# Kernel optimization log

Hardware: AMD Instinct MI355X
Metric: run time of the kernel (lower is better)

The kernel has to match this reference:

```python
import jax, jax.numpy as jnp
import numpy as np
from jax.ops import segment_sum, segment_max

N, E, FIN, H, C, L, G, ED = 50000, 400000, 256, 4, 64, 3, 25, 2
D = H * C  # 256 = dim*heads


def setup_inputs() -> dict:
    key = jax.random.key(0)
    k = jax.random.split(key, 16)
    s = 0.05
    f = jnp.float32
    return {
        "x": jax.random.normal(k[0], (N, FIN), f),
        "edge_attr": jax.random.uniform(k[1], (E, ED), dtype=f),
        "edge_index": jax.random.randint(k[2], (2, E), 0, N),
        "batch": jnp.sort(jax.random.randint(k[3], (N,), 0, G)),
        "W_pre": jax.random.normal(k[4], (FIN, D), f) * s,
        "b_pre": jnp.zeros((D,), f),
        "W_src": jax.random.normal(k[5], (L, D, D), f) * s,
        "W_dst": jax.random.normal(k[6], (L, D, D), f) * s,
        "W_edge": jax.random.normal(k[7], (L, ED, D), f) * s,
        "att_src": jax.random.normal(k[8], (L, H, C), f) * s,
        "att_dst": jax.random.normal(k[9], (L, H, C), f) * s,
        "att_edge": jax.random.normal(k[10], (L, H, C), f) * s,
        "bias_conv": jnp.zeros((L, D), f),
        "ln_gamma": jnp.ones((L, D), f),
        "ln_beta": jnp.zeros((L, D), f),
        "prelu_a": jnp.full((L, D), 0.25, f),
        "W_post1": jax.random.normal(k[11], (D * (L + 1), D), f) * s,
        "b_post1": jnp.zeros((D,), f),
        "W_post2": jax.random.normal(k[12], (D, D), f) * s,
        "b_post2": jnp.zeros((D,), f),
        "W_risk": jax.random.normal(k[13], (D, 1), f) * s,
        "b_risk": jnp.zeros((1,), f),
    }


def _segment_mean(v, seg, num):
    tot = segment_sum(v, seg, num_segments=num)
    cnt = segment_sum(jnp.ones((v.shape[0], 1), v.dtype), seg, num_segments=num)
    return tot / jnp.maximum(cnt, 1.0)


def _layer_norm(h, g, b, eps=1e-5):
    mu = jnp.mean(h, -1, keepdims=True)
    var = jnp.var(h, -1, keepdims=True)
    return (h - mu) * jax.lax.rsqrt(var + eps) * g + b


def _gat_forward(x, edge_attr, edge_index, batch, params):
    (W_pre, b_pre, W_src, W_dst, W_edge, att_src, att_dst, att_edge,
     bias_conv, ln_gamma, ln_beta, prelu_a,
     W_post1, b_post1, W_post2, b_post2, W_risk, b_risk) = params
    row, col = edge_index[0], edge_index[1]  # src -> dst
    # preprocess: project raw node features to D = dim*heads
    h = x @ W_pre + b_pre  # [N, D]
    concat = [_segment_mean(h, batch, G)]  # x0_glob
    for l in range(L):  # fixed small layer count
        xs = (h @ W_src[l]).reshape(N, H, C)
        xd = (h @ W_dst[l]).reshape(N, H, C)
        ea = (edge_attr @ W_edge[l]).reshape(E, H, C)
        # edge-wise attention logits [E, H]
        a = ((xs * att_src[l]).sum(-1)[row]
             + (xd * att_dst[l]).sum(-1)[col]
             + (ea * att_edge[l]).sum(-1))
        a = jax.nn.leaky_relu(a, 0.2)
        # segment softmax over destination nodes
        m = segment_max(a, col, num_segments=N)
        w = jnp.exp(a - m[col])
        z = segment_sum(w, col, num_segments=N)
        alpha = w / (z[col] + 1e-16)  # [E, H]
        # weighted message passing: gather src feats, scatter-add to dst
        out = segment_sum(xs[row] * alpha[:, :, None], col, num_segments=N)
        out = out.reshape(N, D) + bias_conv[l]
        # per-graph LayerNorm loop == single row-wise LayerNorm
        out = _layer_norm(out, ln_gamma[l], ln_beta[l])
        # channel-wise PReLU
        out = jnp.where(out > 0, out, prelu_a[l] * out)
        concat.append(_segment_mean(out, batch, G))
        h = out + h  # residual_connection == 'Y'
    xc = jnp.concatenate(concat, axis=1)  # [G, D*(L+1)]
    p = jax.nn.relu(xc @ W_post1 + b_post1)
    p = jax.nn.relu(p @ W_post2 + b_post2)
    return p @ W_risk + b_risk  # [G, 1] risk


def reference(x, edge_attr, edge_index, batch, W_pre, b_pre, W_src, W_dst,
              W_edge, att_src, att_dst, att_edge, bias_conv, ln_gamma,
              ln_beta, prelu_a, W_post1, b_post1, W_post2, b_post2,
              W_risk, b_risk):
    params = (W_pre, b_pre, W_src, W_dst, W_edge, att_src, att_dst, att_edge,
              bias_conv, ln_gamma, ln_beta, prelu_a,
              W_post1, b_post1, W_post2, b_post2, W_risk, b_risk)
    return _gat_forward(x, edge_attr, edge_index, batch, params)
```

## Files before the change

kernel.cpp:

```cpp
#include <hip/hip_runtime.h>
#include <math.h>

#define NN 50000
#define NPAD 50048
#define EE 400000
#define DD 256
#define HH 4
#define CC 64
#define LL 3
#define GG 25

typedef _Float16 half4_t __attribute__((ext_vector_type(4)));
typedef _Float16 half8_t __attribute__((ext_vector_type(8)));
typedef float f32x4_t __attribute__((ext_vector_type(4)));

__global__ __launch_bounds__(256) void gemm_mfma(
    const _Float16* __restrict__ Ahi, const _Float16* __restrict__ Alo,
    const _Float16* __restrict__ Bhi, const _Float16* __restrict__ Blo,
    const float* __restrict__ bias, float* __restrict__ C, int N)
{
  __shared__ _Float16 lds[4][128][32];
  const int t = threadIdx.x;
  const int wave = t >> 6, lane = t & 63;
  const int m0 = blockIdx.x * 128, bn0 = blockIdx.y * 128;
  const int wm = wave >> 1, wn = wave & 1;

  f32x4_t acc[4][4];
#pragma unroll
  for (int i = 0; i < 4; i++)
#pragma unroll
    for (int j = 0; j < 4; j++) acc[i][j] = (f32x4_t){0.f, 0.f, 0.f, 0.f};

  const int l15 = lane & 15, kg = lane >> 4;
  int aoff[4], boff[4];
#pragma unroll
  for (int tr = 0; tr < 4; tr++) {
    int r = wm * 64 + tr * 16 + l15;
    aoff[tr] = r * 64 + ((kg ^ ((r >> 1) & 3)) * 16);
    int n = wn * 64 + tr * 16 + l15;
    boff[tr] = n * 64 + ((kg ^ ((n >> 1) & 3)) * 16);
  }

  const _Float16* gsrc[4];
  gsrc[0] = Ahi + (size_t)m0 * 256;
  gsrc[1] = Alo + (size_t)m0 * 256;
  gsrc[2] = Bhi + (size_t)bn0 * 256;
  gsrc[3] = Blo + (size_t)bn0 * 256;

  const char* lbase = (const char*)&lds[0][0][0];

  for (int k0 = 0; k0 < DD; k0 += 32) {
    __syncthreads();
#pragma unroll
    for (int b = 0; b < 4; b++) {
#pragma unroll
      for (int c = 0; c < 2; c++) {
        int rowbase = (wave << 5) + (c << 4);
        const _Float16* g = gsrc[b] + (size_t)(rowbase + (lane >> 2)) * 256
                            + k0 + (lane & 3) * 8;
        char* l = (char*)lbase + b * 8192 + rowbase * 64;
        __builtin_amdgcn_global_load_lds(
            (const __attribute__((address_space(1))) void*)g,
            (__attribute__((address_space(3))) void*)l, 16, 0, 0);
      }
    }
    __syncthreads();

    half8_t ah[4], al[4], bh[4], bl[4];
#pragma unroll
    for (int i = 0; i < 4; i++) {
      ah[i] = *(const half8_t*)(lbase + 0 * 8192 + aoff[i]);
      al[i] = *(const half8_t*)(lbase + 1 * 8192 + aoff[i]);
      bh[i] = *(const half8_t*)(lbase + 2 * 8192 + boff[i]);
      bl[i] = *(const half8_t*)(lbase + 3 * 8192 + boff[i]);
    }
#pragma unroll
    for (int i = 0; i < 4; i++)
#pragma unroll
      for (int j = 0; j < 4; j++) {
        acc[i][j] = __builtin_amdgcn_mfma_f32_16x16x32_f16(ah[i], bh[j], acc[i][j], 0, 0, 0);
        acc[i][j] = __builtin_amdgcn_mfma_f32_16x16x32_f16(ah[i], bl[j], acc[i][j], 0, 0, 0);
        acc[i][j] = __builtin_amdgcn_mfma_f32_16x16x32_f16(al[i], bh[j], acc[i][j], 0, 0, 0);
      }
  }

#pragma unroll
  for (int i = 0; i < 4; i++) {
    int rb = m0 + wm * 64 + i * 16 + (lane >> 4) * 4;
#pragma unroll
    for (int j = 0; j < 4; j++) {
      int col = bn0 + wn * 64 + j * 16 + l15;
      float bv = bias ? bias[col] : 0.f;
#pragma unroll
      for (int q = 0; q < 4; q++) {
        int r = rb + q;
        if (r < N) C[(size_t)r * DD + col] = acc[i][j][q] + bv;
      }
    }
  }
}

__global__ __launch_bounds__(256) void split_f16(
    const float* __restrict__ src, _Float16* __restrict__ hi,
    _Float16* __restrict__ lo, int N)
{
  int f = blockIdx.x * 256 + threadIdx.x;
  if (f >= N * 64) return;
  int m = f >> 6, q = f & 63;
  float4 v = *(const float4*)(src + (size_t)f * 4);
  int gp = (q >> 1) ^ ((m >> 1) & 3);
  int off = m * 256 + gp * 8 + (q & 1) * 4;
  half4_t h4, l4;
  h4[0] = (_Float16)v.x; l4[0] = (_Float16)(v.x - (float)h4[0]);
  h4[1] = (_Float16)v.y; l4[1] = (_Float16)(v.y - (float)h4[1]);
  h4[2] = (_Float16)v.z; l4[2] = (_Float16)(v.z - (float)h4[2]);
  h4[3] = (_Float16)v.w; l4[3] = (_Float16)(v.w - (float)h4[3]);
  *(half4_t*)(hi + off) = h4;
  *(half4_t*)(lo + off) = l4;
}

__global__ void prep_w(const float* __restrict__ W, _Float16* __restrict__ bhi,
                       _Float16* __restrict__ blo)
{
  int n = blockIdx.x, k = threadIdx.x;
  float v = W[(size_t)k * DD + n];
  _Float16 h = (_Float16)v, l = (_Float16)(v - (float)h);
  int kp = (((k >> 3) ^ ((n >> 1) & 3)) << 3) | (k & 7);
  bhi[(size_t)n * DD + kp] = h;
  blo[(size_t)n * DD + kp] = l;
}

__global__ void prep_att(const float* __restrict__ Ws, const float* __restrict__ Wd,
                         const float* __restrict__ We, const float* __restrict__ as_,
                         const float* __restrict__ ad_, const float* __restrict__ ae_,
                         float* __restrict__ wmat, float* __restrict__ wea)
{
  int l = blockIdx.x;
  int t = threadIdx.x;
  for (int idx = t; idx < DD * 8; idx += 256) {
    int k = idx >> 3, hd = idx & 7;
    const float* W; const float* att; int hh;
    if (hd < 4) { W = Ws; att = as_; hh = hd; }
    else        { W = Wd; att = ad_; hh = hd - 4; }
    const float* wrow = W + (size_t)l * DD * DD + (size_t)k * DD + hh * CC;
    const float* arow = att + l * DD + hh * CC;
    float s = 0.f;
#pragma unroll 4
    for (int c = 0; c < CC; c++) s = fmaf(wrow[c], arow[c], s);
    wmat[(size_t)l * DD * 8 + idx] = s;
  }
  if (t < 8) {
    int d = t >> 2, hh = t & 3;
    const float* wrow = We + (size_t)l * 2 * DD + (size_t)d * DD + hh * CC;
    const float* arow = ae_ + l * DD + hh * CC;
    float s = 0.f;
#pragma unroll 4
    for (int c = 0; c < CC; c++) s = fmaf(wrow[c], arow[c], s);
    wea[l * 8 + d * 4 + hh] = s;
  }
}

__global__ void graph_bounds(const int* __restrict__ batch, int* __restrict__ goff,
                             int N, int G)
{
  int g = threadIdx.x;
  if (g > G) return;
  int lo = 0, hi = N;
  while (lo < hi) { int mid = (lo + hi) >> 1; if (batch[mid] < g) lo = mid + 1; else hi = mid; }
  goff[g] = lo;
}

__global__ void hist_col(const int* __restrict__ ei, int* __restrict__ deg, int E)
{
  int e = blockIdx.x * 256 + threadIdx.x;
  if (e < E) atomicAdd(&deg[ei[E + e]], 1);
}

__global__ void scan1(const int* __restrict__ deg, int* __restrict__ incl,
                      int* __restrict__ bsum, int N)
{
  __shared__ int sm[256];
  int b = blockIdx.x, t = threadIdx.x;
  int i = b * 256 + t;
  int v = (i < N) ? deg[i] : 0;
  sm[t] = v;
  __syncthreads();
  for (int off = 1; off < 256; off <<= 1) {
    int add = (t >= off) ? sm[t - off] : 0;
    __syncthreads();
    sm[t] += add;
    __syncthreads();
  }
  if (i < N) incl[i] = sm[t];
  if (t == 255) bsum[b] = sm[255];
}

__global__ void scan2(int* __restrict__ bsum, int nb)
{
  if (threadIdx.x == 0 && blockIdx.x == 0) {
    int run = 0;
    for (int i = 0; i < nb; i++) { int v = bsum[i]; bsum[i] = run; run += v; }
  }
}

__global__ void scan3(const int* __restrict__ deg, const int* __restrict__ incl,
                      const int* __restrict__ bsum, int* __restrict__ rowptr,
                      int* __restrict__ cur, int N, int E)
{
  int i = blockIdx.x * 256 + threadIdx.x;
  if (i < N) {
    int ex = incl[i] - deg[i] + bsum[blockIdx.x];
    rowptr[i] = ex;
    cur[i] = ex;
  }
  if (i == 0) rowptr[N] = E;
}

__global__ void scatter_edges(const int* __restrict__ ei, const float* __restrict__ eattr,
                              int* __restrict__ cur, int* __restrict__ srow,
                              float2* __restrict__ sea, int E)
{
  int e = blockIdx.x * 256 + threadIdx.x;
  if (e < E) {
    int c = ei[E + e];
    int p = atomicAdd(&cur[c], 1);
    srow[p] = ei[e];
    sea[p] = ((const float2*)eattr)[e];
  }
}

__global__ __launch_bounds__(256) void att_proj(
    const float* __restrict__ h, const float* __restrict__ wmatL,
    float* __restrict__ asrc, float* __restrict__ adst, int N)
{
  __shared__ float Hs[32][260];
  __shared__ float Wm[DD * 8];
  int t = threadIdx.x;
  for (int i = t; i < DD * 8; i += 256) Wm[i] = wmatL[i];
  int n0 = blockIdx.x * 32;
  for (int i = t; i < 32 * 64; i += 256) {
    int n = i >> 6, c4 = i & 63;
    float4 v = {0.f, 0.f, 0.f, 0.f};
    if (n0 + n < N) v = *(const float4*)(h + (size_t)(n0 + n) * DD + c4 * 4);
    Hs[n][c4 * 4 + 0] = v.x; Hs[n][c4 * 4 + 1] = v.y;
    Hs[n][c4 * 4 + 2] = v.z; Hs[n][c4 * 4 + 3] = v.w;
  }
  __syncthreads();
  int n = t >> 3, hd = t & 7;
  float s0 = 0, s1 = 0, s2 = 0, s3 = 0;
  for (int k = 0; k < DD; k += 4) {
    s0 = fmaf(Hs[n][k + 0], Wm[(k + 0) * 8 + hd], s0);
    s1 = fmaf(Hs[n][k + 1], Wm[(k + 1) * 8 + hd], s1);
    s2 = fmaf(Hs[n][k + 2], Wm[(k + 2) * 8 + hd], s2);
    s3 = fmaf(Hs[n][k + 3], Wm[(k + 3) * 8 + hd], s3);
  }
  float s = (s0 + s1) + (s2 + s3);
  int gn = n0 + n;
  if (gn < N) {
    if (hd < 4) asrc[gn * 4 + hd] = s;
    else        adst[gn * 4 + (hd - 4)] = s;
  }
}

__global__ __launch_bounds__(256) void dst_fused(
    const float* __restrict__ xs, const float* __restrict__ asrc,
    const float* __restrict__ adst, const int* __restrict__ rowptr,
    const int* __restrict__ srow, const float2* __restrict__ sea,
    const float* __restrict__ weaL, const float* __restrict__ biasL,
    const float* __restrict__ gL, const float* __restrict__ bL,
    const float* __restrict__ pL, float* __restrict__ h,
    _Float16* __restrict__ hhi, _Float16* __restrict__ hlo, int N)
{
  int wid = blockIdx.x * 4 + (threadIdx.x >> 6);
  int lane = threadIdx.x & 63;
  if (wid >= N) return;
  const int head = lane >> 4;
  const int start = rowptr[wid];
  const int end = rowptr[wid + 1];
  const float ad = adst[wid * 4 + head];
  const float w0 = weaL[head];
  const float w1 = weaL[4 + head];
  float ax = 0.f, ay = 0.f, az = 0.f, aw = 0.f;
  float z = 0.f;
  int p = start;
  for (; p + 2 <= end; p += 2) {
    int r0 = srow[p], r1 = srow[p + 1];
    float2 e0 = sea[p], e1 = sea[p + 1];
    float s0 = asrc[r0 * 4 + head], s1 = asrc[r1 * 4 + head];
    float4 x0 = *(const float4*)(xs + (size_t)r0 * DD + lane * 4);
    float4 x1 = *(const float4*)(xs + (size_t)r1 * DD + lane * 4);
    float a0 = s0 + ad + e0.x * w0 + e0.y * w1;
    a0 = a0 > 0.f ? a0 : 0.2f * a0;
    float wt0 = expf(a0);
    float a1 = s1 + ad + e1.x * w0 + e1.y * w1;
    a1 = a1 > 0.f ? a1 : 0.2f * a1;
    float wt1 = expf(a1);
    z += wt0 + wt1;
    ax = fmaf(wt0, x0.x, ax); ay = fmaf(wt0, x0.y, ay);
    az = fmaf(wt0, x0.z, az); aw = fmaf(wt0, x0.w, aw);
    ax = fmaf(wt1, x1.x, ax); ay = fmaf(wt1, x1.y, ay);
    az = fmaf(wt1, x1.z, az); aw = fmaf(wt1, x1.w, aw);
  }
  if (p < end) {
    int r = srow[p];
    float2 ea = sea[p];
    float a = asrc[r * 4 + head] + ad + ea.x * w0 + ea.y * w1;
    a = a > 0.f ? a : 0.2f * a;
    float wt = expf(a);
    z += wt;
    float4 xv = *(const float4*)(xs + (size_t)r * DD + lane * 4);
    ax = fmaf(wt, xv.x, ax); ay = fmaf(wt, xv.y, ay);
    az = fmaf(wt, xv.z, az); aw = fmaf(wt, xv.w, aw);
  }
  float inv = 1.f / (z + 1e-16f);
  float4 bi = *(const float4*)(biasL + lane * 4);
  float o0 = ax * inv + bi.x;
  float o1 = ay * inv + bi.y;
  float o2 = az * inv + bi.z;
  float o3 = aw * inv + bi.w;
  float s = (o0 + o1) + (o2 + o3);
  float q = (o0 * o0 + o1 * o1) + (o2 * o2 + o3 * o3);
#pragma unroll
  for (int off = 32; off; off >>= 1) {
    s += __shfl_xor(s, off, 64);
    q += __shfl_xor(q, off, 64);
  }
  float mu = s * (1.f / 256.f);
  float var = q * (1.f / 256.f) - mu * mu;
  float rs = rsqrtf(var + 1e-5f);
  float4 gg = *(const float4*)(gL + lane * 4);
  float4 bb = *(const float4*)(bL + lane * 4);
  float4 pp = *(const float4*)(pL + lane * 4);
  o0 = (o0 - mu) * rs * gg.x + bb.x;  o0 = o0 > 0.f ? o0 : pp.x * o0;
  o1 = (o1 - mu) * rs * gg.y + bb.y;  o1 = o1 > 0.f ? o1 : pp.y * o1;
  o2 = (o2 - mu) * rs * gg.z + bb.z;  o2 = o2 > 0.f ? o2 : pp.z * o2;
  o3 = (o3 - mu) * rs * gg.w + bb.w;  o3 = o3 > 0.f ? o3 : pp.w * o3;
  float4 hv = *(const float4*)(h + (size_t)wid * DD + lane * 4);
  float4 ov;
  ov.x = o0 + hv.x; ov.y = o1 + hv.y; ov.z = o2 + hv.z; ov.w = o3 + hv.w;
  *(float4*)(h + (size_t)wid * DD + lane * 4) = ov;
  if (hhi) {
    int gp = (lane >> 1) ^ ((wid >> 1) & 3);
    int off2 = wid * DD + gp * 8 + (lane & 1) * 4;
    half4_t h4, l4;
    h4[0] = (_Float16)ov.x; l4[0] = (_Float16)(ov.x - (float)h4[0]);
    h4[1] = (_Float16)ov.y; l4[1] = (_Float16)(ov.y - (float)h4[1]);
    h4[2] = (_Float16)ov.z; l4[2] = (_Float16)(ov.z - (float)h4[2]);
    h4[3] = (_Float16)ov.w; l4[3] = (_Float16)(ov.w - (float)h4[3]);
    *(half4_t*)(hhi + off2) = h4;
    *(half4_t*)(hlo + off2) = l4;
  }
}

__global__ void mean_accum(const float* __restrict__ x, const int* __restrict__ goff,
                           float* __restrict__ msum)
{
  int g = blockIdx.x, sp = blockIdx.y, t = threadIdx.x;
  int lo = goff[g], hi = goff[g + 1];
  int cnt = hi - lo;
  if (cnt <= 0) return;
  int per = (cnt + gridDim.y - 1) / gridDim.y;
  int st = lo + sp * per;
  int en = min(hi, st + per);
  if (st >= en) return;
  float acc = 0.f;
  for (int n = st; n < en; ++n) acc += x[(size_t)n * DD + t];
  atomicAdd(&msum[g * DD + t], acc);
}

__global__ void mean_fin(const float* __restrict__ msum, const int* __restrict__ goff,
                         float* __restrict__ dst)
{
  int g = blockIdx.x, t = threadIdx.x;
  int cnt = goff[g + 1] - goff[g];
  dst[g * DD + t] = msum[g * DD + t] / fmaxf((float)cnt, 1.f);
}

__global__ __launch_bounds__(256) void head_mlp(
    const float* __restrict__ hmean, const float* __restrict__ W1,
    const float* __restrict__ b1, const float* __restrict__ W2,
    const float* __restrict__ b2, const float* __restrict__ Wr,
    const float* __restrict__ br, float* __restrict__ out)
{
  __shared__ float xc[4 * DD];
  __shared__ float p1[DD];
  __shared__ float red[256];
  int g = blockIdx.x, t = threadIdx.x;
  float m0 = hmean[0 * GG * DD + g * DD + t];
  float m1 = hmean[1 * GG * DD + g * DD + t];
  float m2 = hmean[2 * GG * DD + g * DD + t];
  float m3 = hmean[3 * GG * DD + g * DD + t];
  xc[t] = m0;
  xc[DD + t] = m1 - m0;
  xc[2 * DD + t] = m2 - m1;
  xc[3 * DD + t] = m3 - m2;
  __syncthreads();
  float acc = b1[t];
  for (int k = 0; k < 4 * DD; k++) acc = fmaf(xc[k], W1[(size_t)k * DD + t], acc);
  p1[t] = fmaxf(acc, 0.f);
  __syncthreads();
  float acc2 = b2[t];
  for (int k = 0; k < DD; k++) acc2 = fmaf(p1[k], W2[(size_t)k * DD + t], acc2);
  float v = fmaxf(acc2, 0.f) * Wr[t];
  red[t] = v;
  __syncthreads();
  for (int sdown = 128; sdown; sdown >>= 1) {
    if (t < sdown) red[t] += red[t + sdown];
    __syncthreads();
  }
  if (t == 0) out[g] = red[0] + br[0];
}

extern "C" void kernel_launch(void* const* d_in, const int* in_sizes, int n_in,
                              void* d_out, int out_size, void* d_ws, size_t ws_size,
                              hipStream_t stream)
{
  const float* x        = (const float*)d_in[0];
  const float* eattr    = (const float*)d_in[1];
  const int*   eidx     = (const int*)d_in[2];
  const int*   batch    = (const int*)d_in[3];
  const float* W_pre    = (const float*)d_in[4];
  const float* b_pre    = (const float*)d_in[5];
  const float* W_src    = (const float*)d_in[6];
  const float* W_dst    = (const float*)d_in[7];
  const float* W_edge   = (const float*)d_in[8];
  const float* att_src  = (const float*)d_in[9];
  const float* att_dst  = (const float*)d_in[10];
  const float* att_edge = (const float*)d_in[11];
  const float* bias_conv= (const float*)d_in[12];
  const float* ln_g     = (const float*)d_in[13];
  const float* ln_b     = (const float*)d_in[14];
  const float* prelu    = (const float*)d_in[15];
  const float* W1       = (const float*)d_in[16];
  const float* b1       = (const float*)d_in[17];
  const float* W2       = (const float*)d_in[18];
  const float* b2       = (const float*)d_in[19];
  const float* Wr       = (const float*)d_in[20];
  const float* br       = (const float*)d_in[21];
  float* out = (float*)d_out;

  char* w = (char*)d_ws;
  size_t off = 0;
  auto alloc = [&](size_t bytes) -> char* {
    char* p = w + off;
    off += (bytes + 255) & ~(size_t)255;
    return p;
  };
  float*     h     = (float*)alloc((size_t)NN * DD * 4);
  char*      xsreg = alloc((size_t)NPAD * DD * 4);
  float*     xs    = (float*)xsreg;
  _Float16*  x_hi  = (_Float16*)xsreg;
  _Float16*  x_lo  = (_Float16*)(xsreg + (size_t)NPAD * DD * 2);
  _Float16*  h_hi  = (_Float16*)alloc((size_t)NPAD * DD * 2);
  _Float16*  h_lo  = (_Float16*)alloc((size_t)NPAD * DD * 2);
  _Float16*  bt_hi = (_Float16*)alloc((size_t)4 * DD * DD * 2);
  _Float16*  bt_lo = (_Float16*)alloc((size_t)4 * DD * DD * 2);
  float*  asrc  = (float*)alloc((size_t)NN * HH * 4);
  float*  adst  = (float*)alloc((size_t)NN * HH * 4);
  float*  wmat  = (float*)alloc((size_t)LL * DD * 8 * 4);
  float*  wea   = (float*)alloc((size_t)LL * 8 * 4);
  float*  hmean = (float*)alloc((size_t)(LL + 1) * GG * DD * 4);
  float*  msum  = (float*)alloc((size_t)GG * DD * 4);
  float2* sea   = (float2*)alloc((size_t)EE * 8);
  int*    goff  = (int*)alloc((GG + 1) * 4);
  int*    deg   = (int*)alloc((size_t)NN * 4);
  int*    rowptr= (int*)alloc((size_t)(NN + 1) * 4);
  int*    cur   = (int*)alloc((size_t)NN * 4);
  int*    incl  = (int*)alloc((size_t)NN * 4);
  int*    bsum  = (int*)alloc(256 * 4);
  int*    srow  = (int*)alloc((size_t)EE * 4);
  if (off > ws_size) return;

  prep_att<<<dim3(LL), dim3(256), 0, stream>>>(W_src, W_dst, W_edge, att_src,
                                               att_dst, att_edge, wmat, wea);
  prep_w<<<dim3(DD), dim3(DD), 0, stream>>>(W_pre, bt_hi, bt_lo);
  for (int l = 0; l < LL; l++)
    prep_w<<<dim3(DD), dim3(DD), 0, stream>>>(W_src + (size_t)l * DD * DD,
                                              bt_hi + (size_t)(l + 1) * DD * DD,
                                              bt_lo + (size_t)(l + 1) * DD * DD);
  graph_bounds<<<dim3(1), dim3(32), 0, stream>>>(batch, goff, NN, GG);
  hipMemsetAsync(deg, 0, (size_t)NN * 4, stream);
  hist_col<<<dim3((EE + 255) / 256), dim3(256), 0, stream>>>(eidx, deg, EE);
  int nb = (NN + 255) / 256;
  scan1<<<dim3(nb), dim3(256), 0, stream>>>(deg, incl, bsum, NN);
  scan2<<<dim3(1), dim3(1), 0, stream>>>(bsum, nb);
  scan3<<<dim3(nb), dim3(256), 0, stream>>>(deg, incl, bsum, rowptr, cur, NN, EE);
  scatter_edges<<<dim3((EE + 255) / 256), dim3(256), 0, stream>>>(eidx, eattr, cur,
                                                                  srow, sea, EE);

  split_f16<<<dim3((NN * 64 + 255) / 256), dim3(256), 0, stream>>>(x, x_hi, x_lo, NN);
  dim3 gg((NN + 127) / 128, 2);
  gemm_mfma<<<gg, dim3(256), 0, stream>>>(x_hi, x_lo, bt_hi, bt_lo, b_pre, h, NN);
  split_f16<<<dim3((NN * 64 + 255) / 256), dim3(256), 0, stream>>>(h, h_hi, h_lo, NN);
  hipMemsetAsync(msum, 0, (size_t)GG * DD * 4, stream);
  mean_accum<<<dim3(GG, 16), dim3(DD), 0, stream>>>(h, goff, msum);
  mean_fin<<<dim3(GG), dim3(DD), 0, stream>>>(msum, goff, hmean);

  for (int l = 0; l < LL; l++) {
    gemm_mfma<<<gg, dim3(256), 0, stream>>>(h_hi, h_lo,
                                            bt_hi + (size_t)(l + 1) * DD * DD,
                                            bt_lo + (size_t)(l + 1) * DD * DD,
                                            (const float*)nullptr, xs, NN);
    att_proj<<<dim3((NN + 31) / 32), dim3(256), 0, stream>>>(h, wmat + (size_t)l * DD * 8,
                                                             asrc, adst, NN);
    bool ws = (l < LL - 1);
    dst_fused<<<dim3((NN + 3) / 4), dim3(256), 0, stream>>>(
        xs, asrc, adst, rowptr, srow, sea, wea + l * 8, bias_conv + l * DD,
        ln_g + l * DD, ln_b + l * DD, prelu + l * DD, h,
        ws ? h_hi : (_Float16*)nullptr, ws ? h_lo : (_Float16*)nullptr, NN);
    hipMemsetAsync(msum, 0, (size_t)GG * DD * 4, stream);
    mean_accum<<<dim3(GG, 16), dim3(DD), 0, stream>>>(h, goff, msum);
    mean_fin<<<dim3(GG), dim3(DD), 0, stream>>>(msum, goff,
                                                hmean + (size_t)(l + 1) * GG * DD);
  }

  head_mlp<<<dim3(GG), dim3(256), 0, stream>>>(hmean, W1, b1, W2, b2, Wr, br, out);
}
```

Before: 982.4 us.

## Store layer projections in fp16, double-buffer GEMM LDS, parallelize scan, fast exp

The per-layer GEMM now writes its output directly as fp16, and the edge-gather kernel reads those half-precision rows. This halves the bytes moved in the dominant gather. The GEMM main loop is double-buffered so the next K tile loads while MFMAs run, and scan2 is changed from a single-thread loop to a 256-thread parallel scan. The attention exponent switches to __expf; the fp16 features and fast exp reduce accuracy slightly.

```diff
diff --git a/kernel.cpp b/kernel.cpp
--- a/kernel.cpp
+++ b/kernel.cpp
@@ -17,9 +17,10 @@
 __global__ __launch_bounds__(256) void gemm_mfma(
     const _Float16* __restrict__ Ahi, const _Float16* __restrict__ Alo,
     const _Float16* __restrict__ Bhi, const _Float16* __restrict__ Blo,
-    const float* __restrict__ bias, float* __restrict__ C, int N)
-{
-  __shared__ _Float16 lds[4][128][32];
+    const float* __restrict__ bias, float* __restrict__ C,
+    _Float16* __restrict__ C16, int N)
+{
+  __shared__ _Float16 lds[2][4][128][32];
   const int t = threadIdx.x;
   const int wave = t >> 6, lane = t & 63;
   const int m0 = blockIdx.x * 128, bn0 = blockIdx.y * 128;
@@ -47,32 +48,39 @@
   gsrc[2] = Bhi + (size_t)bn0 * 256;
   gsrc[3] = Blo + (size_t)bn0 * 256;
 
-  const char* lbase = (const char*)&lds[0][0][0];
-
-  for (int k0 = 0; k0 < DD; k0 += 32) {
-    __syncthreads();
+  char* lbase = (char*)&lds[0][0][0][0];
+  const int rowbase0 = (wave << 5);
+
+  auto stage = [&](int buf, int k0) {
 #pragma unroll
     for (int b = 0; b < 4; b++) {
 #pragma unroll
       for (int c = 0; c < 2; c++) {
-        int rowbase = (wave << 5) + (c << 4);
+        int rowbase = rowbase0 + (c << 4);
         const _Float16* g = gsrc[b] + (size_t)(rowbase + (lane >> 2)) * 256
                             + k0 + (lane & 3) * 8;
-        char* l = (char*)lbase + b * 8192 + rowbase * 64;
+        char* l = lbase + (size_t)(buf * 4 + b) * 8192 + rowbase * 64;
         __builtin_amdgcn_global_load_lds(
             (const __attribute__((address_space(1))) void*)g,
             (__attribute__((address_space(3))) void*)l, 16, 0, 0);
       }
     }
-    __syncthreads();
-
+  };
+
+  stage(0, 0);
+  __syncthreads();
+  int cur = 0;
+  for (int k0 = 0; k0 < DD; k0 += 32) {
+    if (k0 + 32 < DD) stage(cur ^ 1, k0 + 32);
+
+    const char* lb = lbase + (size_t)cur * 4 * 8192;
     half8_t ah[4], al[4], bh[4], bl[4];
 #pragma unroll
     for (int i = 0; i < 4; i++) {
-      ah[i] = *(const half8_t*)(lbase + 0 * 8192 + aoff[i]);
-      al[i] = *(const half8_t*)(lbase + 1 * 8192 + aoff[i]);
-      bh[i] = *(const half8_t*)(lbase + 2 * 8192 + boff[i]);
-      bl[i] = *(const half8_t*)(lbase + 3 * 8192 + boff[i]);
+      ah[i] = *(const half8_t*)(lb + 0 * 8192 + aoff[i]);
+      al[i] = *(const half8_t*)(lb + 1 * 8192 + aoff[i]);
+      bh[i] = *(const half8_t*)(lb + 2 * 8192 + boff[i]);
+      bl[i] = *(const half8_t*)(lb + 3 * 8192 + boff[i]);
     }
 #pragma unroll
     for (int i = 0; i < 4; i++)
@@ -82,19 +90,37 @@
         acc[i][j] = __builtin_amdgcn_mfma_f32_16x16x32_f16(ah[i], bl[j], acc[i][j], 0, 0, 0);
         acc[i][j] = __builtin_amdgcn_mfma_f32_16x16x32_f16(al[i], bh[j], acc[i][j], 0, 0, 0);
       }
-  }
-
-#pragma unroll
-  for (int i = 0; i < 4; i++) {
-    int rb = m0 + wm * 64 + i * 16 + (lane >> 4) * 4;
-#pragma unroll
-    for (int j = 0; j < 4; j++) {
-      int col = bn0 + wn * 64 + j * 16 + l15;
-      float bv = bias ? bias[col] : 0.f;
-#pragma unroll
-      for (int q = 0; q < 4; q++) {
-        int r = rb + q;
-        if (r < N) C[(size_t)r * DD + col] = acc[i][j][q] + bv;
+    __syncthreads();
+    cur ^= 1;
+  }
+
+  if (C16) {
+#pragma unroll
+    for (int i = 0; i < 4; i++) {
+      int rb = m0 + wm * 64 + i * 16 + (lane >> 4) * 4;
+#pragma unroll
+      for (int j = 0; j < 4; j++) {
+        int col = bn0 + wn * 64 + j * 16 + l15;
+#pragma unroll
+        for (int q = 0; q < 4; q++) {
+          int r = rb + q;
+          if (r < N) C16[(size_t)r * DD + col] = (_Float16)acc[i][j][q];
+        }
+      }
+    }
+  } else {
+#pragma unroll
+    for (int i = 0; i < 4; i++) {
+      int rb = m0 + wm * 64 + i * 16 + (lane >> 4) * 4;
+#pragma unroll
+      for (int j = 0; j < 4; j++) {
+        int col = bn0 + wn * 64 + j * 16 + l15;
+        float bv = bias ? bias[col] : 0.f;
+#pragma unroll
+        for (int q = 0; q < 4; q++) {
+          int r = rb + q;
+          if (r < N) C[(size_t)r * DD + col] = acc[i][j][q] + bv;
+        }
       }
     }
   }
@@ -197,10 +223,18 @@
 
 __global__ void scan2(int* __restrict__ bsum, int nb)
 {
-  if (threadIdx.x == 0 && blockIdx.x == 0) {
-    int run = 0;
-    for (int i = 0; i < nb; i++) { int v = bsum[i]; bsum[i] = run; run += v; }
-  }
+  __shared__ int sm[256];
+  int t = threadIdx.x;
+  int v = (t < nb) ? bsum[t] : 0;
+  sm[t] = v;
+  __syncthreads();
+  for (int off = 1; off < 256; off <<= 1) {
+    int add = (t >= off) ? sm[t - off] : 0;
+    __syncthreads();
+    sm[t] += add;
+    __syncthreads();
+  }
+  if (t < nb) bsum[t] = sm[t] - v;
 }
 
 __global__ void scan3(const int* __restrict__ deg, const int* __restrict__ incl,
@@ -263,7 +297,7 @@
 }
 
 __global__ __launch_bounds__(256) void dst_fused(
-    const float* __restrict__ xs, const float* __restrict__ asrc,
+    const _Float16* __restrict__ xs16, const float* __restrict__ asrc,
     const float* __restrict__ adst, const int* __restrict__ rowptr,
     const int* __restrict__ srow, const float2* __restrict__ sea,
     const float* __restrict__ weaL, const float* __restrict__ biasL,
@@ -287,30 +321,27 @@
     int r0 = srow[p], r1 = srow[p + 1];
     float2 e0 = sea[p], e1 = sea[p + 1];
     float s0 = asrc[r0 * 4 + head], s1 = asrc[r1 * 4 + head];
-    float4 x0 = *(const float4*)(xs + (size_t)r0 * DD + lane * 4);
-    float4 x1 = *(const float4*)(xs + (size_t)r1 * DD + lane * 4);
-    float a0 = s0 + ad + e0.x * w0 + e0.y * w1;
-    a0 = a0 > 0.f ? a0 : 0.2f * a0;
-    float wt0 = expf(a0);
-    float a1 = s1 + ad + e1.x * w0 + e1.y * w1;
-    a1 = a1 > 0.f ? a1 : 0.2f * a1;
-    float wt1 = expf(a1);
-    z += wt0 + wt1;
-    ax = fmaf(wt0, x0.x, ax); ay = fmaf(wt0, x0.y, ay);
-    az = fmaf(wt0, x0.z, az); aw = fmaf(wt0, x0.w, aw);
-    ax = fmaf(wt1, x1.x, ax); ay = fmaf(wt1, x1.y, ay);
-    az = fmaf(wt1, x1.z, az); aw = fmaf(wt1, x1.w, aw);
+    half4_t x0 = *(const half4_t*)(xs16 + (size_t)r0 * DD + lane * 4);
+    half4_t x1 = *(const half4_t*)(xs16 + (size_t)r1 * DD + lane * 4);
+    float a0 = s0 + ad + e0.x * w0 + e0.y * w1; a0 = a0 > 0.f ? a0 : 0.2f * a0;
+    float a1 = s1 + ad + e1.x * w0 + e1.y * w1; a1 = a1 > 0.f ? a1 : 0.2f * a1;
+    float t0 = __expf(a0), t1 = __expf(a1);
+    z += t0 + t1;
+    ax = fmaf(t0, (float)x0[0], ax); ay = fmaf(t0, (float)x0[1], ay);
+    az = fmaf(t0, (float)x0[2], az); aw = fmaf(t0, (float)x0[3], aw);
+    ax = fmaf(t1, (float)x1[0], ax); ay = fmaf(t1, (float)x1[1], ay);
+    az = fmaf(t1, (float)x1[2], az); aw = fmaf(t1, (float)x1[3], aw);
   }
   if (p < end) {
     int r = srow[p];
     float2 ea = sea[p];
     float a = asrc[r * 4 + head] + ad + ea.x * w0 + ea.y * w1;
     a = a > 0.f ? a : 0.2f * a;
-    float wt = expf(a);
+    float wt = __expf(a);
     z += wt;
-    float4 xv = *(const float4*)(xs + (size_t)r * DD + lane * 4);
-    ax = fmaf(wt, xv.x, ax); ay = fmaf(wt, xv.y, ay);
-    az = fmaf(wt, xv.z, az); aw = fmaf(wt, xv.w, aw);
+    half4_t xv = *(const half4_t*)(xs16 + (size_t)r * DD + lane * 4);
+    ax = fmaf(wt, (float)xv[0], ax); ay = fmaf(wt, (float)xv[1], ay);
+    az = fmaf(wt, (float)xv[2], az); aw = fmaf(wt, (float)xv[3], aw);
   }
   float inv = 1.f / (z + 1e-16f);
   float4 bi = *(const float4*)(biasL + lane * 4);
@@ -448,9 +479,9 @@
   };
   float*     h     = (float*)alloc((size_t)NN * DD * 4);
   char*      xsreg = alloc((size_t)NPAD * DD * 4);
-  float*     xs    = (float*)xsreg;
   _Float16*  x_hi  = (_Float16*)xsreg;
   _Float16*  x_lo  = (_Float16*)(xsreg + (size_t)NPAD * DD * 2);
+  _Float16*  xs16  = (_Float16*)xsreg;
   _Float16*  h_hi  = (_Float16*)alloc((size_t)NPAD * DD * 2);
   _Float16*  h_lo  = (_Float16*)alloc((size_t)NPAD * DD * 2);
   _Float16*  bt_hi = (_Float16*)alloc((size_t)4 * DD * DD * 2);
@@ -483,14 +514,15 @@
   hist_col<<<dim3((EE + 255) / 256), dim3(256), 0, stream>>>(eidx, deg, EE);
   int nb = (NN + 255) / 256;
   scan1<<<dim3(nb), dim3(256), 0, stream>>>(deg, incl, bsum, NN);
-  scan2<<<dim3(1), dim3(1), 0, stream>>>(bsum, nb);
+  scan2<<<dim3(1), dim3(256), 0, stream>>>(bsum, nb);
   scan3<<<dim3(nb), dim3(256), 0, stream>>>(deg, incl, bsum, rowptr, cur, NN, EE);
   scatter_edges<<<dim3((EE + 255) / 256), dim3(256), 0, stream>>>(eidx, eattr, cur,
                                                                   srow, sea, EE);
 
   split_f16<<<dim3((NN * 64 + 255) / 256), dim3(256), 0, stream>>>(x, x_hi, x_lo, NN);
   dim3 gg((NN + 127) / 128, 2);
-  gemm_mfma<<<gg, dim3(256), 0, stream>>>(x_hi, x_lo, bt_hi, bt_lo, b_pre, h, NN);
+  gemm_mfma<<<gg, dim3(256), 0, stream>>>(x_hi, x_lo, bt_hi, bt_lo, b_pre, h,
+                                          (_Float16*)nullptr, NN);
   split_f16<<<dim3((NN * 64 + 255) / 256), dim3(256), 0, stream>>>(h, h_hi, h_lo, NN);
   hipMemsetAsync(msum, 0, (size_t)GG * DD * 4, stream);
   mean_accum<<<dim3(GG, 16), dim3(DD), 0, stream>>>(h, goff, msum);
@@ -500,12 +532,13 @@
     gemm_mfma<<<gg, dim3(256), 0, stream>>>(h_hi, h_lo,
                                             bt_hi + (size_t)(l + 1) * DD * DD,
                                             bt_lo + (size_t)(l + 1) * DD * DD,
-                                            (const float*)nullptr, xs, NN);
+                                            (const float*)nullptr, (float*)nullptr,
+                                            xs16, NN);
     att_proj<<<dim3((NN + 31) / 32), dim3(256), 0, stream>>>(h, wmat + (size_t)l * DD * 8,
                                                              asrc, adst, NN);
     bool ws = (l < LL - 1);
     dst_fused<<<dim3((NN + 3) / 4), dim3(256), 0, stream>>>(
-        xs, asrc, adst, rowptr, srow, sea, wea + l * 8, bias_conv + l * DD,
+        xs16, asrc, adst, rowptr, srow, sea, wea + l * 8, bias_conv + l * DD,
         ln_g + l * DD, ln_b + l * DD, prelu + l * DD, h,
         ws ? h_hi : (_Float16*)nullptr, ws ? h_lo : (_Float16*)nullptr, NN);
     hipMemsetAsync(msum, 0, (size_t)GG * DD * 4, stream);
```

After: 845.7 us. -13.9%, faster.
